# Performance work log

Hardware: AMD Instinct MI355X
Metric: run time of the kernel (lower is better)

## Reference

```python
import jax, jax.numpy as jnp
import numpy as np

E = 1024
H = 16
D = E // H  # 64


def setup_inputs() -> dict:
    key = jax.random.key(0)
    ks = jax.random.split(key, 8)
    B, Lq, Lkv = 2, 2048, 2048
    scale = 1.0 / np.sqrt(E)  # xavier-ish scale for square weights
    return {
        "query": jax.random.normal(ks[0], (B, Lq, E), dtype=jnp.float32),
        "key_value": jax.random.normal(ks[1], (B, Lkv, E), dtype=jnp.float32),
        "mask": jax.random.randint(ks[2], (B, Lkv), 0, 2, dtype=jnp.int32),
        "Wq": jax.random.normal(ks[3], (E, E), dtype=jnp.float32) * scale,
        "bq": jnp.zeros((E,), dtype=jnp.float32),
        "Wk": jax.random.normal(ks[4], (E, E), dtype=jnp.float32) * scale,
        "bk": jnp.zeros((E,), dtype=jnp.float32),
        "Wv": jax.random.normal(ks[5], (E, E), dtype=jnp.float32) * scale,
        "bv": jnp.zeros((E,), dtype=jnp.float32),
        "Wo": jax.random.normal(ks[6], (E, E), dtype=jnp.float32) * scale,
        "bo": jnp.zeros((E,), dtype=jnp.float32),
    }


def reference(query, key_value, mask, Wq, bq, Wk, bk, Wv, bv, Wo, bo):
    B, Lq, _ = query.shape
    Lkv = key_value.shape[1]
    # torch nn.Linear: x @ W.T + b
    Q = (query @ Wq.T + bq).reshape(B, Lq, H, D)
    K = (key_value @ Wk.T + bk).reshape(B, Lkv, H, D)
    V = (key_value @ Wv.T + bv).reshape(B, Lkv, H, D)
    scores = jnp.einsum("bqhd,bkhd->bhqk", Q, K) / jnp.sqrt(jnp.float32(D))
    scores = jnp.where(mask[:, None, None, :] == 0, -jnp.inf, scores)
    probs = jax.nn.softmax(scores, axis=-1)  # [B,H,Lq,Lkv]
    context = jnp.einsum("bhqk,bkhd->bqhd", probs, V).reshape(B, Lq, E)
    return context @ Wo.T + bo
```

## Files before the change

kernel.cpp:

```cpp
#include <hip/hip_runtime.h>


typedef unsigned short u16;
typedef unsigned int u32;
typedef __attribute__((ext_vector_type(2))) float f32x2;
typedef __attribute__((ext_vector_type(4))) float f32x4;
typedef __attribute__((ext_vector_type(16))) float f32x16;
typedef __attribute__((ext_vector_type(8))) short s16x8;
typedef __attribute__((ext_vector_type(4))) u16 u16x4;
typedef __attribute__((ext_vector_type(4))) u32 u32x4;

#define C_SCALE 0.18033688011112042f
#define NEGBIG -30000.0f

__device__ __forceinline__ u16 f2bf(float f) {
  u32 u = __builtin_bit_cast(u32, f);
  u += 0x7FFFu + ((u >> 16) & 1u);
  return (u16)(u >> 16);
}

__device__ __forceinline__ float exp2_fast(float x) {
  float r;
  asm("v_exp_f32 %0, %1" : "=v"(r) : "v"(x));
  return r;
}

typedef const __attribute__((address_space(1))) u32 GAS;
typedef __attribute__((address_space(3))) u32 LAS;
__device__ __forceinline__ void g2l16(const u16* g, u16* l) {
  __builtin_amdgcn_global_load_lds((GAS*)g, (LAS*)l, 16, 0, 0);
}

__device__ __forceinline__ f32x16 z16() {
  f32x16 v;
#pragma unroll
  for (int i = 0; i < 16; ++i) v[i] = 0.f;
  return v;
}

__global__ void cvt_all(const float* __restrict__ q, u16* __restrict__ qb,
                        const float* __restrict__ w0, u16* __restrict__ o0,
                        const float* __restrict__ w1, u16* __restrict__ o1,
                        const float* __restrict__ w2, u16* __restrict__ o2,
                        const float* __restrict__ w3, u16* __restrict__ o3) {
  const int tid = threadIdx.x;
  const float* s;
  u16* d;
  int i;
  if (blockIdx.y == 0) {
    s = q; d = qb;
    i = blockIdx.x * 256 + tid;
  } else {
    const int wsel = blockIdx.x >> 10;
    s = wsel == 0 ? w0 : wsel == 1 ? w1 : wsel == 2 ? w2 : w3;
    d = wsel == 0 ? o0 : wsel == 1 ? o1 : wsel == 2 ? o2 : o3;
    i = (blockIdx.x & 1023) * 256 + tid;
  }
  f32x4 v = ((const f32x4*)s)[i];
  u16x4 o;
  o[0] = f2bf(v[0]); o[1] = f2bf(v[1]); o[2] = f2bf(v[2]); o[3] = f2bf(v[3]);
  ((u16x4*)d)[i] = o;
}

__global__ void scan_mask(const int* __restrict__ mask, int* __restrict__ srcidx,
                          float* __restrict__ madd2c, int* __restrict__ nkv_a,
                          int* __restrict__ nkvp_a, int* __restrict__ nt_a) {
  const int b = blockIdx.x;
  const int tid = threadIdx.x;
  __shared__ int part[256];
  int loc[8], mv[8];
  int s = 0;
  const int base = b * 2048 + tid * 8;
#pragma unroll
  for (int i = 0; i < 8; ++i) {
    mv[i] = mask[base + i];
    loc[i] = s;
    s += (mv[i] != 0);
  }
  part[tid] = s;
  __syncthreads();
  for (int off = 1; off < 256; off <<= 1) {
    int v = (tid >= off) ? part[tid - off] : 0;
    __syncthreads();
    part[tid] += v;
    __syncthreads();
  }
  const int excl = part[tid] - s;
  const int total = part[255];
#pragma unroll
  for (int i = 0; i < 8; ++i)
    if (mv[i]) srcidx[b * 2048 + excl + loc[i]] = tid * 8 + i;
#pragma unroll
  for (int i = 0; i < 8; ++i) {
    const int j = tid * 8 + i;
    madd2c[b * 2048 + j] = (j < total) ? 0.f : NEGBIG;
  }
  if (tid == 0) {
    const int nkvp = ((total + 63) >> 6) << 6;
    nkv_a[b] = total;
    nkvp_a[b] = nkvp;
    nt_a[b] = nkvp >> 6;
  }
}

__global__ void gather_kv(const float* __restrict__ keyv, const int* __restrict__ srcidx,
                          const int* __restrict__ nkv_a, const int* __restrict__ nkvp_a,
                          u16* __restrict__ kvc) {
  const int j = blockIdx.x;
  const int b = blockIdx.y;
  const int tid = threadIdx.x;
  const int nkv = nkv_a[b];
  if (j < nkv) {
    const int src = srcidx[b * 2048 + j];
    const f32x4 v = *(const f32x4*)&keyv[((size_t)(b * 2048 + src)) * 1024 + tid * 4];
    u16x4 o;
    o[0] = f2bf(v[0]); o[1] = f2bf(v[1]); o[2] = f2bf(v[2]); o[3] = f2bf(v[3]);
    *(u16x4*)&kvc[((size_t)(b * 2048 + j)) * 1024 + tid * 4] = o;
  } else if (j < nkvp_a[b]) {
    u16x4 z = {0, 0, 0, 0};
    *(u16x4*)&kvc[((size_t)(b * 2048 + j)) * 1024 + tid * 4] = z;
  }
}

struct Jobs {
  const u16* A[3];
  const u16* W[3];
  const float* bias[3];
  void* out[3];
  const int* mlim[3];
  int mode[3];
};

__global__ __launch_bounds__(512, 4) void gemm8(Jobs jb) {
  const int z = blockIdx.z;
  const u16* __restrict__ A = jb.A[z];
  const u16* __restrict__ W = jb.W[z];
  const float* __restrict__ bias = jb.bias[z];
  void* __restrict__ out = jb.out[z];
  const int mode = jb.mode[z];
  const int m0 = blockIdx.y * 128, n0 = blockIdx.x * 128;
  const int* mlim = jb.mlim[z];
  if (mlim && ((m0 & 2047) >= mlim[m0 >> 11])) return;

  __shared__ u16 smem[32768];
  const int tid = threadIdx.x;
  const int w = tid >> 6, lane = tid & 63;
  const int wr = w >> 1, wc = w & 1;
  const int l15 = lane & 15, l4 = lane >> 4;
  const int srow = lane >> 3, sslot = lane & 7;

  f32x4 acc[2][4];
#pragma unroll
  for (int m = 0; m < 2; ++m)
#pragma unroll
    for (int n = 0; n < 4; ++n) acc[m][n] = (f32x4){0.f, 0.f, 0.f, 0.f};

  auto STAGE = [&](int buf, int k0) {
    u16* As = smem + buf * 16384;
    u16* Bs = As + 8192;
#pragma unroll
    for (int it = 0; it < 4; ++it) {
      const int rbase = (w & 3) * 32 + it * 8;
      const int r = rbase + srow;
      const int ca = ((sslot ^ (r & 7)) << 3);
      if (w < 4) g2l16(A + (size_t)(m0 + r) * 1024 + k0 + ca, &As[rbase * 64]);
      else       g2l16(W + (size_t)(n0 + r) * 1024 + k0 + ca, &Bs[rbase * 64]);
    }
  };

  STAGE(0, 0);
  __syncthreads();
  int cur = 0;
  for (int k0 = 0; k0 < 1024; k0 += 64) {
    if (k0 < 960) STAGE(cur ^ 1, k0 + 64);
    const u16* As = smem + cur * 16384;
    const u16* Bs = As + 8192;

    s16x8 af[2][2], bf[4][2];
#pragma unroll
    for (int m = 0; m < 2; ++m) {
      const int row = wr * 32 + m * 16 + l15;
#pragma unroll
      for (int kk = 0; kk < 2; ++kk) {
        const int slot = (kk * 4 + l4) ^ (row & 7);
        af[m][kk] = *(const s16x8*)&As[row * 64 + slot * 8];
      }
    }
#pragma unroll
    for (int n = 0; n < 4; ++n) {
      const int row = wc * 64 + n * 16 + l15;
#pragma unroll
      for (int kk = 0; kk < 2; ++kk) {
        const int slot = (kk * 4 + l4) ^ (row & 7);
        bf[n][kk] = *(const s16x8*)&Bs[row * 64 + slot * 8];
      }
    }
#pragma unroll
    for (int m = 0; m < 2; ++m)
#pragma unroll
      for (int n = 0; n < 4; ++n)
#pragma unroll
        for (int kk = 0; kk < 2; ++kk)
          acc[m][n] = __builtin_amdgcn_mfma_f32_16x16x32_bf16(af[m][kk], bf[n][kk],
                                                              acc[m][n], 0, 0, 0);
    __syncthreads();
    cur ^= 1;
  }

  if (mode != 1) {
#pragma unroll
    for (int n = 0; n < 4; ++n) {
      const int col = n0 + wc * 64 + n * 16 + l15;
      const float bv = bias[col];
#pragma unroll
      for (int m = 0; m < 2; ++m) {
        const int rowb = m0 + wr * 32 + m * 16 + l4 * 4;
#pragma unroll
        for (int j = 0; j < 4; ++j) {
          const float v = acc[m][n][j] + bv;
          if (mode == 2) ((float*)out)[(size_t)(rowb + j) * 1024 + col] = v;
          else           ((u16*)out)[(size_t)(rowb + j) * 1024 + col] = f2bf(v);
        }
      }
    }
  } else {
    u16* T = smem;
#pragma unroll
    for (int n = 0; n < 4; ++n) {
      const int col = wc * 64 + n * 16 + l15;
      const float bv = bias[n0 + col];
#pragma unroll
      for (int m = 0; m < 2; ++m) {
        const int rowb = wr * 32 + m * 16 + l4 * 4;
        u16x4 v;
#pragma unroll
        for (int j = 0; j < 4; ++j) v[j] = f2bf(acc[m][n][j] + bv);
        *(u16x4*)&T[col * 128 + (rowb ^ ((col & 7) * 8))] = v;
      }
    }
    __syncthreads();
    u16* Vt = (u16*)out;
#pragma unroll
    for (int pass = 0; pass < 4; ++pass) {
      const int c = pass * 32 + (tid >> 4);
      const int slot = tid & 15;
      const s16x8 v = *(const s16x8*)&T[c * 128 + ((slot * 8) ^ ((c & 7) * 8))];
      const int cg = n0 + c, h = cg >> 6, d = cg & 63;
      const int rg = m0 + slot * 8, b = rg >> 11, rr = rg & 2047;
      *(s16x8*)&Vt[(((size_t)(b * 16 + h) * 64) + d) * 2048 + rr] = v;
    }
  }
}

__global__ __launch_bounds__(256, 4) void attn_fwd(const u16* __restrict__ Qp,
                                                   const u16* __restrict__ Kp,
                                                   const u16* __restrict__ Vt,
                                                   const float* __restrict__ madd2c,
                                                   const int* __restrict__ nt_a,
                                                   u16* __restrict__ ctx) {
  __shared__ alignas(16) u16 smem[16384];
  __shared__ float lb[4][32];
  const int tid = threadIdx.x;
  const int w = tid >> 6, lane = tid & 63;
  const int l31 = lane & 31, h5 = lane >> 5;
  const int qs = w & 1, half = w >> 1;
  const int q0 = blockIdx.x * 64;
  const int head = blockIdx.y, b = blockIdx.z;
  const int srow = lane >> 3, sslot = lane & 7;
  const int vrow = lane >> 2, vslot = lane & 3;
  const int nt = nt_a[b];
  const int kvbase = half * (nt << 5);

  const u16* qbase = Qp + ((size_t)(b * 2048 + q0 + qs * 32 + l31)) * 1024 + head * 64 + h5 * 8;
  s16x8 qf[4];
#pragma unroll
  for (int k = 0; k < 4; ++k) qf[k] = *(const s16x8*)(qbase + k * 16);

  f32x16 oa = z16(), ob = z16();
  float l_run = 0.f;

  auto STAGE = [&](int buf, int t) {
    u16* Ks = &smem[(buf * 2 + half) * 4096];
    u16* Vs = Ks + 2048;
    const int kv0 = kvbase + t * 32;
#pragma unroll
    for (int it = 0; it < 2; ++it) {
      const int rbase = qs * 16 + it * 8;
      const int r = rbase + srow;
      const int ca = ((sslot ^ (r & 7)) << 3);
      g2l16(Kp + (size_t)(b * 2048 + kv0 + r) * 1024 + head * 64 + ca, &Ks[rbase * 64]);
    }
#pragma unroll
    for (int it = 0; it < 2; ++it) {
      const int rb = qs * 32 + it * 16;
      const int rv = rb + vrow;
      const int key = (rv & 3) ^ ((rv >> 2) & 3);
      const int cav = ((vslot ^ key) << 3);
      g2l16(Vt + (((size_t)(b * 16 + head) * 64) + rv) * 2048 + kv0 + cav, &Vs[rb * 32]);
    }
  };

  STAGE(0, 0);
  __syncthreads();
  int cur = 0;

  for (int t = 0; t < nt; ++t) {
    if (t < nt - 1) STAGE(cur ^ 1, t + 1);
    const u16* Ks = &smem[(cur * 2 + half) * 4096];
    const u16* Vs = Ks + 2048;

    const float* mptr = madd2c + b * 2048 + kvbase + t * 32 + h5 * 4;
    f32x4 mk[4];
#pragma unroll
    for (int c = 0; c < 4; ++c) mk[c] = *(const f32x4*)(mptr + c * 8);

    f32x16 s0 = z16();
    __builtin_amdgcn_s_setprio(1);
#pragma unroll
    for (int ks = 0; ks < 4; ++ks) {
      const int cu = (ks * 16 + h5 * 8) ^ ((l31 & 7) * 8);
      const s16x8 kf = *(const s16x8*)&Ks[l31 * 64 + cu];
      s0 = __builtin_amdgcn_mfma_f32_32x32x16_bf16(kf, qf[ks], s0, 0, 0, 0);
    }
    __builtin_amdgcn_s_setprio(0);

    float p[16];
#pragma unroll
    for (int c = 0; c < 4; ++c)
#pragma unroll
      for (int e = 0; e < 4; ++e)
        p[c * 4 + e] = exp2_fast(fmaf(s0[c * 4 + e], C_SCALE, mk[c][e]));

    float t8[8];
#pragma unroll
    for (int i = 0; i < 8; ++i) t8[i] = p[i] + p[i + 8];
#pragma unroll
    for (int i = 0; i < 4; ++i) t8[i] += t8[i + 4];
    float ps = (t8[0] + t8[1]) + (t8[2] + t8[3]);
    ps += __shfl_xor(ps, 32, 64);
    l_run += ps;

    u32 pk[8];
#pragma unroll
    for (int j = 0; j < 8; ++j) {
      u32 d;
      asm("v_cvt_pk_bf16_f32 %0, %1, %2" : "=v"(d) : "v"(p[2 * j]), "v"(p[2 * j + 1]));
      pk[j] = d;
    }
    s16x8 pf[2];
#pragma unroll
    for (int kk = 0; kk < 2; ++kk) {
      u32 a0 = pk[kk * 4 + 0], a1 = pk[kk * 4 + 1];
      u32 b0 = pk[kk * 4 + 2], b1 = pk[kk * 4 + 3];
      asm("v_permlane32_swap_b32 %0, %1" : "+v"(a0), "+v"(b0));
      asm("v_permlane32_swap_b32 %0, %1" : "+v"(a1), "+v"(b1));
      u32x4 fv; fv[0] = a0; fv[1] = a1; fv[2] = b0; fv[3] = b1;
      pf[kk] = __builtin_bit_cast(s16x8, fv);
    }

    const int vkey = (l31 & 3) ^ ((l31 >> 2) & 3);
    __builtin_amdgcn_s_setprio(1);
#pragma unroll
    for (int kk = 0; kk < 2; ++kk) {
      const int c = ((kk * 2 + h5) ^ vkey) << 3;
      const s16x8 vf0 = *(const s16x8*)&Vs[l31 * 32 + c];
      const s16x8 vf1 = *(const s16x8*)&Vs[(32 + l31) * 32 + c];
      oa = __builtin_amdgcn_mfma_f32_32x32x16_bf16(vf0, pf[kk], oa, 0, 0, 0);
      ob = __builtin_amdgcn_mfma_f32_32x32x16_bf16(vf1, pf[kk], ob, 0, 0, 0);
    }
    __builtin_amdgcn_s_setprio(0);

    __syncthreads();
    cur ^= 1;
  }

  lb[w][l31] = l_run;
  __syncthreads();
  const float l_o = lb[w ^ 2][l31];
  const float inv = 1.f / (l_run + l_o);

  float* Of = (float*)smem;
  const int okey = ((l31 & 7) << 3) ^ ((l31 >> 3) << 2);
  if (w >= 2) {
    const int qb2 = (w - 2) * 2048;
#pragma unroll
    for (int dblk = 0; dblk < 2; ++dblk)
#pragma unroll
      for (int g = 0; g < 4; ++g) {
        const int d0 = dblk * 32 + 8 * g + 4 * h5;
        f32x4 v;
#pragma unroll
        for (int e = 0; e < 4; ++e) v[e] = (dblk ? ob[g * 4 + e] : oa[g * 4 + e]);
        *(f32x4*)&Of[qb2 + l31 * 64 + (d0 ^ okey)] = v;
      }
  }
  __syncthreads();
  if (w < 2) {
    u16* Ot = &smem[8192 + qs * 2048];
#pragma unroll
    for (int dblk = 0; dblk < 2; ++dblk)
#pragma unroll
      for (int g = 0; g < 4; ++g) {
        const int d0 = dblk * 32 + 8 * g + 4 * h5;
        const f32x4 ofv = *(const f32x4*)&Of[qs * 2048 + l31 * 64 + (d0 ^ okey)];
        u16x4 v4;
#pragma unroll
        for (int e = 0; e < 4; ++e) {
          const float fin = ((dblk ? ob[g * 4 + e] : oa[g * 4 + e]) + ofv[e]) * inv;
          v4[e] = f2bf(fin);
        }
        *(u16x4*)&Ot[l31 * 64 + (d0 ^ ((l31 & 7) * 8))] = v4;
      }
#pragma unroll
    for (int pass = 0; pass < 4; ++pass) {
      const int row = pass * 8 + srow;
      const s16x8 v = *(const s16x8*)&Ot[row * 64 + ((sslot * 8) ^ ((row & 7) * 8))];
      *(s16x8*)(ctx + ((size_t)(b * 2048 + q0 + qs * 32 + row)) * 1024 + head * 64 + sslot * 8) = v;
    }
  }
}

extern "C" void kernel_launch(void* const* d_in, const int* in_sizes, int n_in,
                              void* d_out, int out_size, void* d_ws, size_t ws_size,
                              hipStream_t stream) {
  const float* query = (const float*)d_in[0];
  const float* keyv = (const float*)d_in[1];
  const int* mask = (const int*)d_in[2];
  const float* Wq = (const float*)d_in[3];
  const float* bq = (const float*)d_in[4];
  const float* Wk = (const float*)d_in[5];
  const float* bk = (const float*)d_in[6];
  const float* Wv = (const float*)d_in[7];
  const float* bv = (const float*)d_in[8];
  const float* Wo = (const float*)d_in[9];
  const float* bo = (const float*)d_in[10];

  const size_t NTOK = (size_t)4096 * 1024;
  const size_t NW = (size_t)1024 * 1024;
  u16* p = (u16*)d_ws;
  u16* qb = p;  p += NTOK;
  u16* wqb = p; p += NW;
  u16* wkb = p; p += NW;
  u16* wvb = p; p += NW;
  u16* wob = p; p += NW;
  u16* Qp = p;  p += NTOK;
  u16* Kp = p;  p += NTOK;
  u16* Vt = p;  p += NTOK;
  u16* kvc = p; p += NTOK;
  float* madd2c = (float*)p; p += 8192;
  int* srcidx = (int*)p; p += 8192;
  int* meta = (int*)p;
  int* nkv_a = meta;
  int* nkvp_a = meta + 2;
  int* nt_a = meta + 4;
  u16* ctx = qb;

  cvt_all<<<dim3(4096, 2), 256, 0, stream>>>(query, qb, Wq, wqb, Wk, wkb, Wv, wvb, Wo, wob);
  scan_mask<<<2, 256, 0, stream>>>(mask, srcidx, madd2c, nkv_a, nkvp_a, nt_a);
  gather_kv<<<dim3(2048, 2), 256, 0, stream>>>(keyv, srcidx, nkv_a, nkvp_a, kvc);

  Jobs pj;
  pj.A[0] = qb;  pj.W[0] = wqb; pj.bias[0] = bq; pj.out[0] = Qp; pj.mode[0] = 0; pj.mlim[0] = nullptr;
  pj.A[1] = kvc; pj.W[1] = wkb; pj.bias[1] = bk; pj.out[1] = Kp; pj.mode[1] = 0; pj.mlim[1] = nkvp_a;
  pj.A[2] = kvc; pj.W[2] = wvb; pj.bias[2] = bv; pj.out[2] = Vt; pj.mode[2] = 1; pj.mlim[2] = nkvp_a;
  gemm8<<<dim3(8, 32, 3), 512, 0, stream>>>(pj);

  attn_fwd<<<dim3(32, 16, 2), 256, 0, stream>>>(Qp, Kp, Vt, madd2c, nt_a, ctx);

  Jobs oj;
  oj.A[0] = ctx; oj.W[0] = wob; oj.bias[0] = bo; oj.out[0] = d_out; oj.mode[0] = 2; oj.mlim[0] = nullptr;
  oj.A[1] = ctx; oj.W[1] = wob; oj.bias[1] = bo; oj.out[1] = d_out; oj.mode[1] = 2; oj.mlim[1] = nullptr;
  oj.A[2] = ctx; oj.W[2] = wob; oj.bias[2] = bo; oj.out[2] = d_out; oj.mode[2] = 2; oj.mlim[2] = nullptr;
  gemm8<<<dim3(8, 32, 1), 512, 0, stream>>>(oj);
}
```

Before: 103.1 us.

## Load K/V fragments directly from global memory, drop LDS staging in attention

```diff
diff --git a/kernel.cpp b/kernel.cpp
--- a/kernel.cpp
+++ b/kernel.cpp
@@ -252,88 +252,71 @@
   }
 }
 
-__global__ __launch_bounds__(256, 4) void attn_fwd(const u16* __restrict__ Qp,
+__global__ __launch_bounds__(128, 4) void attn_fwd(const u16* __restrict__ Qp,
                                                    const u16* __restrict__ Kp,
                                                    const u16* __restrict__ Vt,
                                                    const float* __restrict__ madd2c,
                                                    const int* __restrict__ nt_a,
                                                    u16* __restrict__ ctx) {
-  __shared__ alignas(16) u16 smem[16384];
-  __shared__ float lb[4][32];
+  __shared__ alignas(16) float Of[32 * 64];
+  __shared__ alignas(16) u16 Ot[32 * 64];
+  __shared__ float lb[2][32];
   const int tid = threadIdx.x;
   const int w = tid >> 6, lane = tid & 63;
   const int l31 = lane & 31, h5 = lane >> 5;
-  const int qs = w & 1, half = w >> 1;
-  const int q0 = blockIdx.x * 64;
-  const int head = blockIdx.y, b = blockIdx.z;
   const int srow = lane >> 3, sslot = lane & 7;
-  const int vrow = lane >> 2, vslot = lane & 3;
+
+  const int p = blockIdx.x;
+  const int bh = (p & 7) * 4 + ((p >> 3) & 3);
+  const int qg = p >> 5;
+  const int b = bh >> 4, head = bh & 15;
+  const int q0 = qg * 32;
   const int nt = nt_a[b];
-  const int kvbase = half * (nt << 5);
-
-  const u16* qbase = Qp + ((size_t)(b * 2048 + q0 + qs * 32 + l31)) * 1024 + head * 64 + h5 * 8;
+  const int kvbase = w * (nt << 5);
+
+  const u16* qbase = Qp + ((size_t)(b * 2048 + q0 + l31)) * 1024 + head * 64 + h5 * 8;
   s16x8 qf[4];
 #pragma unroll
   for (int k = 0; k < 4; ++k) qf[k] = *(const s16x8*)(qbase + k * 16);
+
+  const u16* kbase = Kp + ((size_t)(b * 2048 + kvbase + l31)) * 1024 + head * 64 + h5 * 8;
+  const u16* vbase0 = Vt + (((size_t)(b * 16 + head) * 64) + l31) * 2048 + kvbase + h5 * 8;
+  const u16* vbase1 = vbase0 + (size_t)32 * 2048;
+  const float* mbase = madd2c + b * 2048 + kvbase + h5 * 4;
 
   f32x16 oa = z16(), ob = z16();
   float l_run = 0.f;
 
-  auto STAGE = [&](int buf, int t) {
-    u16* Ks = &smem[(buf * 2 + half) * 4096];
-    u16* Vs = Ks + 2048;
-    const int kv0 = kvbase + t * 32;
-#pragma unroll
-    for (int it = 0; it < 2; ++it) {
-      const int rbase = qs * 16 + it * 8;
-      const int r = rbase + srow;
-      const int ca = ((sslot ^ (r & 7)) << 3);
-      g2l16(Kp + (size_t)(b * 2048 + kv0 + r) * 1024 + head * 64 + ca, &Ks[rbase * 64]);
-    }
-#pragma unroll
-    for (int it = 0; it < 2; ++it) {
-      const int rb = qs * 32 + it * 16;
-      const int rv = rb + vrow;
-      const int key = (rv & 3) ^ ((rv >> 2) & 3);
-      const int cav = ((vslot ^ key) << 3);
-      g2l16(Vt + (((size_t)(b * 16 + head) * 64) + rv) * 2048 + kv0 + cav, &Vs[rb * 32]);
-    }
-  };
-
-  STAGE(0, 0);
-  __syncthreads();
-  int cur = 0;
-
   for (int t = 0; t < nt; ++t) {
-    if (t < nt - 1) STAGE(cur ^ 1, t + 1);
-    const u16* Ks = &smem[(cur * 2 + half) * 4096];
-    const u16* Vs = Ks + 2048;
-
-    const float* mptr = madd2c + b * 2048 + kvbase + t * 32 + h5 * 4;
+    const int kv0 = t * 32;
+
+    const u16* kp = kbase + (size_t)kv0 * 1024;
+    s16x8 kf[4];
+#pragma unroll
+    for (int ks = 0; ks < 4; ++ks) kf[ks] = *(const s16x8*)(kp + ks * 16);
+
+    const float* mp = mbase + kv0;
     f32x4 mk[4];
 #pragma unroll
-    for (int c = 0; c < 4; ++c) mk[c] = *(const f32x4*)(mptr + c * 8);
+    for (int c = 0; c < 4; ++c) mk[c] = *(const f32x4*)(mp + c * 8);
 
     f32x16 s0 = z16();
     __builtin_amdgcn_s_setprio(1);
 #pragma unroll
-    for (int ks = 0; ks < 4; ++ks) {
-      const int cu = (ks * 16 + h5 * 8) ^ ((l31 & 7) * 8);
-      const s16x8 kf = *(const s16x8*)&Ks[l31 * 64 + cu];
-      s0 = __builtin_amdgcn_mfma_f32_32x32x16_bf16(kf, qf[ks], s0, 0, 0, 0);
-    }
+    for (int ks = 0; ks < 4; ++ks)
+      s0 = __builtin_amdgcn_mfma_f32_32x32x16_bf16(kf[ks], qf[ks], s0, 0, 0, 0);
     __builtin_amdgcn_s_setprio(0);
 
-    float p[16];
+    float pv[16];
 #pragma unroll
     for (int c = 0; c < 4; ++c)
 #pragma unroll
       for (int e = 0; e < 4; ++e)
-        p[c * 4 + e] = exp2_fast(fmaf(s0[c * 4 + e], C_SCALE, mk[c][e]));
+        pv[c * 4 + e] = exp2_fast(fmaf(s0[c * 4 + e], C_SCALE, mk[c][e]));
 
     float t8[8];
 #pragma unroll
-    for (int i = 0; i < 8; ++i) t8[i] = p[i] + p[i + 8];
+    for (int i = 0; i < 8; ++i) t8[i] = pv[i] + pv[i + 8];
 #pragma unroll
     for (int i = 0; i < 4; ++i) t8[i] += t8[i + 4];
     float ps = (t8[0] + t8[1]) + (t8[2] + t8[3]);
@@ -344,7 +327,7 @@
 #pragma unroll
     for (int j = 0; j < 8; ++j) {
       u32 d;
-      asm("v_cvt_pk_bf16_f32 %0, %1, %2" : "=v"(d) : "v"(p[2 * j]), "v"(p[2 * j + 1]));
+      asm("v_cvt_pk_bf16_f32 %0, %1, %2" : "=v"(d) : "v"(pv[2 * j]), "v"(pv[2 * j + 1]));
       pk[j] = d;
     }
     s16x8 pf[2];
@@ -358,31 +341,26 @@
       pf[kk] = __builtin_bit_cast(s16x8, fv);
     }
 
-    const int vkey = (l31 & 3) ^ ((l31 >> 2) & 3);
+    const u16* vp0 = vbase0 + kv0;
+    const u16* vp1 = vbase1 + kv0;
     __builtin_amdgcn_s_setprio(1);
 #pragma unroll
     for (int kk = 0; kk < 2; ++kk) {
-      const int c = ((kk * 2 + h5) ^ vkey) << 3;
-      const s16x8 vf0 = *(const s16x8*)&Vs[l31 * 32 + c];
-      const s16x8 vf1 = *(const s16x8*)&Vs[(32 + l31) * 32 + c];
+      const s16x8 vf0 = *(const s16x8*)(vp0 + kk * 16);
+      const s16x8 vf1 = *(const s16x8*)(vp1 + kk * 16);
       oa = __builtin_amdgcn_mfma_f32_32x32x16_bf16(vf0, pf[kk], oa, 0, 0, 0);
       ob = __builtin_amdgcn_mfma_f32_32x32x16_bf16(vf1, pf[kk], ob, 0, 0, 0);
     }
     __builtin_amdgcn_s_setprio(0);
-
-    __syncthreads();
-    cur ^= 1;
   }
 
   lb[w][l31] = l_run;
   __syncthreads();
-  const float l_o = lb[w ^ 2][l31];
+  const float l_o = lb[w ^ 1][l31];
   const float inv = 1.f / (l_run + l_o);
 
-  float* Of = (float*)smem;
   const int okey = ((l31 & 7) << 3) ^ ((l31 >> 3) << 2);
-  if (w >= 2) {
-    const int qb2 = (w - 2) * 2048;
+  if (w == 1) {
 #pragma unroll
     for (int dblk = 0; dblk < 2; ++dblk)
 #pragma unroll
@@ -391,18 +369,17 @@
         f32x4 v;
 #pragma unroll
         for (int e = 0; e < 4; ++e) v[e] = (dblk ? ob[g * 4 + e] : oa[g * 4 + e]);
-        *(f32x4*)&Of[qb2 + l31 * 64 + (d0 ^ okey)] = v;
+        *(f32x4*)&Of[l31 * 64 + (d0 ^ okey)] = v;
       }
   }
   __syncthreads();
-  if (w < 2) {
-    u16* Ot = &smem[8192 + qs * 2048];
+  if (w == 0) {
 #pragma unroll
     for (int dblk = 0; dblk < 2; ++dblk)
 #pragma unroll
       for (int g = 0; g < 4; ++g) {
         const int d0 = dblk * 32 + 8 * g + 4 * h5;
-        const f32x4 ofv = *(const f32x4*)&Of[qs * 2048 + l31 * 64 + (d0 ^ okey)];
+        const f32x4 ofv = *(const f32x4*)&Of[l31 * 64 + (d0 ^ okey)];
         u16x4 v4;
 #pragma unroll
         for (int e = 0; e < 4; ++e) {
@@ -411,11 +388,14 @@
         }
         *(u16x4*)&Ot[l31 * 64 + (d0 ^ ((l31 & 7) * 8))] = v4;
       }
+  }
+  __syncthreads();
+  if (w == 0) {
 #pragma unroll
     for (int pass = 0; pass < 4; ++pass) {
       const int row = pass * 8 + srow;
       const s16x8 v = *(const s16x8*)&Ot[row * 64 + ((sslot * 8) ^ ((row & 7) * 8))];
-      *(s16x8*)(ctx + ((size_t)(b * 2048 + q0 + qs * 32 + row)) * 1024 + head * 64 + sslot * 8) = v;
+      *(s16x8*)(ctx + ((size_t)(b * 2048 + q0 + row)) * 1024 + head * 64 + sslot * 8) = v;
     }
   }
 }
@@ -465,7 +445,7 @@
   pj.A[2] = kvc; pj.W[2] = wvb; pj.bias[2] = bv; pj.out[2] = Vt; pj.mode[2] = 1; pj.mlim[2] = nkvp_a;
   gemm8<<<dim3(8, 32, 3), 512, 0, stream>>>(pj);
 
-  attn_fwd<<<dim3(32, 16, 2), 256, 0, stream>>>(Qp, Kp, Vt, madd2c, nt_a, ctx);
+  attn_fwd<<<2048, 128, 0, stream>>>(Qp, Kp, Vt, madd2c, nt_a, ctx);
 
   Jobs oj;
   oj.A[0] = ctx; oj.W[0] = wob; oj.bias[0] = bo; oj.out[0] = d_out; oj.mode[0] = 2; oj.mlim[0] = nullptr;
```

After: 139.6 us. 1.35x slower.
